# Optimization experiments

Measured on AMD Instinct MI355X. Metric: run time of the kernel, lower is better.

Reference implementation:

```python
import jax, jax.numpy as jnp
import numpy as np

EPS = 1e-5

def _conv(x, w, pad, groups=1):
    return jax.lax.conv_general_dilated(
        x, w, window_strides=(1, 1), padding=[(pad, pad), (pad, pad)],
        dimension_numbers=('NCHW', 'OIHW', 'NCHW'), feature_group_count=groups)

def _bn(x, g, b, m, v):
    # inference batch-norm, per-channel
    s = g * jax.lax.rsqrt(v + EPS)
    return x * s[None, :, None, None] + (b - m * s)[None, :, None, None]

def setup_inputs() -> dict:
    key = jax.random.key(0)
    ks = jax.random.split(key, 20)
    B, C, H, W = 32, 128, 64, 64
    cs = C // 2  # c_split = 64
    d = {
        'x': jax.random.normal(ks[0], (B, C, H, W), jnp.float32),
        'weights': jax.random.uniform(ks[1], (B, 2), jnp.float32),
        'indices': jax.random.randint(ks[2], (B, 2), 0, 4, jnp.int32),
        # expert 0: Conv(cs -> C, k=3, p=1) + BN + SiLU
        'e0_w': jax.random.normal(ks[3], (C, cs, 3, 3), jnp.float32) * 0.05,
        'e0_g': jax.random.uniform(ks[4], (C,), jnp.float32, 0.5, 1.5),
        'e0_b': jax.random.normal(ks[5], (C,), jnp.float32) * 0.1,
        'e0_m': jax.random.normal(ks[6], (C,), jnp.float32) * 0.1,
        'e0_v': jax.random.uniform(ks[7], (C,), jnp.float32, 0.5, 1.5),
        # expert 1: depthwise 5x5 (cs, groups=cs) -> 1x1 (cs -> C) -> BN -> SiLU
        'e1_dw': jax.random.normal(ks[8], (cs, 1, 5, 5), jnp.float32) * 0.05,
        'e1_pw': jax.random.normal(ks[9], (C, cs, 1, 1), jnp.float32) * 0.05,
        'e1_g': jax.random.uniform(ks[10], (C,), jnp.float32, 0.5, 1.5),
        'e1_b': jax.random.normal(ks[11], (C,), jnp.float32) * 0.1,
        'e1_m': jax.random.normal(ks[12], (C,), jnp.float32) * 0.1,
        'e1_v': jax.random.uniform(ks[13], (C,), jnp.float32, 0.5, 1.5),
        # expert 2: GhostConv(C -> C): cv1 = Conv(C, C//2, 3), cv2 = Conv(C//2, C//2, 5, groups=C//2)
        'e2a_w': jax.random.normal(ks[14], (cs, C, 3, 3), jnp.float32) * 0.05,
        'e2a_g': jax.random.uniform(ks[15], (cs,), jnp.float32, 0.5, 1.5),
        'e2a_b': jax.random.normal(ks[16], (cs,), jnp.float32) * 0.1,
        'e2a_m': jax.random.normal(ks[17], (cs,), jnp.float32) * 0.1,
        'e2a_v': jax.random.uniform(ks[18], (cs,), jnp.float32, 0.5, 1.5),
        'e2b_w': jax.random.normal(ks[19], (cs, 1, 5, 5), jnp.float32) * 0.05,
    }
    ks2 = jax.random.split(jax.random.key(1), 4)
    d['e2b_g'] = jax.random.uniform(ks2[0], (cs,), jnp.float32, 0.5, 1.5)
    d['e2b_b'] = jax.random.normal(ks2[1], (cs,), jnp.float32) * 0.1
    d['e2b_m'] = jax.random.normal(ks2[2], (cs,), jnp.float32) * 0.1
    d['e2b_v'] = jax.random.uniform(ks2[3], (cs,), jnp.float32, 0.5, 1.5)
    return d

def _forward(x, weights, indices,
             e0_w, e0_g, e0_b, e0_m, e0_v,
             e1_dw, e1_pw, e1_g, e1_b, e1_m, e1_v,
             e2a_w, e2a_g, e2a_b, e2a_m, e2a_v,
             e2b_w, e2b_g, e2b_b, e2b_m, e2b_v):
    C = x.shape[1]
    cs = C // 2
    x_rgb, x_ir = x[:, :cs], x[:, cs:]
    # expert outputs computed densely over the whole batch, masked combine below
    e0 = jax.nn.silu(_bn(_conv(x_rgb, e0_w, pad=1), e0_g, e0_b, e0_m, e0_v))
    e1 = jax.nn.silu(_bn(_conv(_conv(x_ir, e1_dw, pad=2, groups=cs), e1_pw, pad=0),
                         e1_g, e1_b, e1_m, e1_v))
    g1 = jax.nn.silu(_bn(_conv(x, e2a_w, pad=1), e2a_g, e2a_b, e2a_m, e2a_v))
    g2 = jax.nn.silu(_bn(_conv(g1, e2b_w, pad=2, groups=cs), e2b_g, e2b_b, e2b_m, e2b_v))
    e2 = jnp.concatenate([g1, g2], axis=1)
    out = jnp.zeros_like(x)
    K = indices.shape[1]
    for k in range(K):  # small fixed top-k loop
        idx = indices[:, k][:, None, None, None]          # [B,1,1,1]
        w = weights[:, k][:, None, None, None]            # [B,1,1,1]
        out = out + jnp.where(idx == 0, e0 * w, 0.0)
        out = out + jnp.where(idx == 1, e1 * w, 0.0)
        out = out + jnp.where(idx == 2, e2 * w, 0.0)
        out = out + jnp.where(idx == 3, x * 0.1, 0.0)
    return out

def reference(x, weights, indices,
              e0_w, e0_g, e0_b, e0_m, e0_v,
              e1_dw, e1_pw, e1_g, e1_b, e1_m, e1_v,
              e2a_w, e2a_g, e2a_b, e2a_m, e2a_v,
              e2b_w, e2b_g, e2b_b, e2b_m, e2b_v):
    return _forward(x, weights, indices,
                    e0_w, e0_g, e0_b, e0_m, e0_v,
                    e1_dw, e1_pw, e1_g, e1_b, e1_m, e1_v,
                    e2a_w, e2a_g, e2a_b, e2a_m, e2a_v,
                    e2b_w, e2b_g, e2b_b, e2b_m, e2b_v)
```

## Files before the change

kernel.cpp:

```cpp
#include <hip/hip_runtime.h>

#define B_  32
#define C_  128
#define CS  64
#define H_  64
#define W_  64
#define HW  (H_*W_)

typedef __attribute__((ext_vector_type(8))) short bf16x8_t;
typedef __attribute__((ext_vector_type(4))) float f32x4_t;
typedef unsigned short u16;
typedef unsigned int   u32;

__device__ __forceinline__ float silu_f(float v) { return v / (1.f + __expf(-v)); }

__device__ __forceinline__ u16 f2bf(float f) {
    u32 u = __float_as_uint(f);
    u = (u + 0x7FFFu + ((u >> 16) & 1u)) >> 16;
    return (u16)u;
}
__device__ __forceinline__ float bf2f(u16 u) {
    return __uint_as_float(((u32)u) << 16);
}
__device__ __forceinline__ u32 cvtpk(float a, float b) {
    u32 r;
    asm("v_cvt_pk_bf16_f32 %0, %1, %2" : "=v"(r) : "v"(a), "v"(b));
    return r;
}

__device__ __forceinline__ void get_coeffs(const float* __restrict__ wts,
                                           const int* __restrict__ idxs, int b,
                                           float& c0, float& c1, float& c2, float& cid) {
    int   i0 = idxs[b*2+0], i1 = idxs[b*2+1];
    float w0 = wts[b*2+0],  w1 = wts[b*2+1];
    c0  = (i0==0?w0:0.f)   + (i1==0?w1:0.f);
    c1  = (i0==1?w0:0.f)   + (i1==1?w1:0.f);
    c2  = (i0==2?w0:0.f)   + (i1==2?w1:0.f);
    cid = (i0==3?0.1f:0.f) + (i1==3?0.1f:0.f);
}

__global__ __launch_bounds__(256) void k_prep(
    const float* __restrict__ e0w, const float* __restrict__ e2aw, const float* __restrict__ e1pw,
    u16* __restrict__ Wt0f, u16* __restrict__ Wt2f, u16* __restrict__ Wt1f)
{
    const int i0 = blockIdx.x*256 + threadIdx.x, stride = gridDim.x*256;
    for (int i = i0; i < 73728; i += stride) {
        int j = i&7, lane = (i>>3)&63, cog = (i>>9)&7, kc = (i>>12)&1, tap = i>>13;
        int co = cog*16 + (lane&15), ci = kc*32 + (lane>>4)*8 + j;
        Wt0f[i] = f2bf(e0w[(size_t)(co*64 + ci)*9 + tap]);
    }
    for (int i = i0; i < 73728; i += stride) {
        int j = i&7, lane = (i>>3)&63, cog = (i>>9)&3, kc = (i>>11)&3, tap = i>>13;
        int co = cog*16 + (lane&15), ci = kc*32 + (lane>>4)*8 + j;
        Wt2f[i] = f2bf(e2aw[(size_t)(co*128 + ci)*9 + tap]);
    }
    for (int i = i0; i < 8192; i += stride) {
        int j = i&7, lane = (i>>3)&63, cog = (i>>9)&7, kc = (i>>12)&1;
        int co = cog*16 + (lane&15), ci = kc*32 + (lane>>4)*8 + j;
        Wt1f[i] = f2bf(e1pw[(size_t)co*64 + ci]);
    }
}

__device__ __forceinline__ void stage_x(
    const float* __restrict__ xb,
    char* lin, int orow0, int t)
{
    f32x4_t V0[8], V1[8];
    #pragma unroll
    for (int k = 0; k < 8; ++k) {
        const int u = t + k*256;
        const int quad = u & 15, r = (u >> 4) & 3, cp = u >> 6;
        const int hh = orow0 - 1 + r;
        const int hcl = (hh < 0) ? 0 : ((hh > 63) ? 63 : hh);
        const float* p0 = xb + (size_t)(2*cp)*HW + hcl*64 + quad*4;
        asm volatile("global_load_dwordx4 %0, %1, off" : "=v"(V0[k]) : "v"(p0));
        asm volatile("global_load_dwordx4 %0, %1, off" : "=v"(V1[k]) : "v"(p0 + HW));
    }
    asm volatile("s_waitcnt vmcnt(0)" ::: "memory");
    __builtin_amdgcn_sched_barrier(0);
    #pragma unroll
    for (int k = 0; k < 8; ++k) {
        const int u = t + k*256;
        const int quad = u & 15, r = (u >> 4) & 3, cp = u >> 6;
        const int hh = orow0 - 1 + r;
        const bool ok = (hh >= 0 && hh < H_);
        #pragma unroll
        for (int j = 0; j < 4; ++j) {
            const int p = r*66 + quad*4 + j + 1;
            const u32 a = ((u32)p*128 + (u32)cp*4) ^ (((u32)(p & 7)) << 4);
            float f0 = ok ? V0[k][j] : 0.f;
            float f1 = ok ? V1[k][j] : 0.f;
            *(u32*)(lin + a) = cvtpk(f0, f1);
        }
    }
    {
        const int cp = t & 31, side = (t >> 5) & 1, r = t >> 6;
        const int p = r*66 + side*65;
        const u32 a = ((u32)p*128 + (u32)cp*4) ^ (((u32)(p & 7)) << 4);
        *(u32*)(lin + a) = 0u;
    }
}

template<int NCF, int NPF, int TK, int COUT>
__device__ __forceinline__ void conv_pass(
    const char* lin, const u16* __restrict__ wb, int koff,
    int rbase, int pxbase, int l15, int kg,
    f32x4_t (&acc)[NCF][NPF])
{
    bf16x8_t A0[NCF], A1[NCF], A2[NCF];

    auto issueA = [&](int i, bf16x8_t (&dst)[NCF]) {
        const int tap = i >> 1, kcl = i & 1;
        const u16* wt = wb + (size_t)((tap*TK + koff + kcl)*(COUT/16))*512;
        #pragma unroll
        for (int cf = 0; cf < NCF; ++cf)
            asm volatile("global_load_dwordx4 %0, %1, off"
                         : "=v"(dst[cf]) : "v"(wt + ((size_t)cf << 9)));
    };
    auto ldsB = [&](int i, int pf) -> bf16x8_t {
        const int tap = i >> 1, kcl = i & 1;
        const int dh = tap / 3, dwp = tap % 3;
        const int p = (rbase + dh)*66 + pxbase + pf*16 + l15 + dwp;
        u32 a = (u32)p*128 + (u32)kcl*64 + (u32)kg*16;
        a ^= ((u32)(p & 7)) << 4;
        return *(const bf16x8_t*)(lin + a);
    };

    issueA(0, A0);
    issueA(1, A1);
    #pragma unroll
    for (int i = 0; i < 18; ++i) {
        if (i + 2 < 18) {
            const int s = (i + 2) % 3;
            if (s == 0)      issueA(i + 2, A0);
            else if (s == 1) issueA(i + 2, A1);
            else             issueA(i + 2, A2);
        }
        if (i < 16)       asm volatile("s_waitcnt vmcnt(8)" ::: "memory");
        else if (i == 16) asm volatile("s_waitcnt vmcnt(4)" ::: "memory");
        else              asm volatile("s_waitcnt vmcnt(0)" ::: "memory");
        __builtin_amdgcn_sched_barrier(0);
        bf16x8_t* ac = (i % 3 == 0) ? A0 : ((i % 3 == 1) ? A1 : A2);
        #pragma unroll
        for (int pf = 0; pf < NPF; ++pf) {
            bf16x8_t bfr = ldsB(i, pf);
            #pragma unroll
            for (int cf = 0; cf < NCF; ++cf)
                acc[cf][pf] = __builtin_amdgcn_mfma_f32_16x16x32_bf16(ac[cf], bfr, acc[cf][pf], 0, 0, 0);
        }
    }
}

__global__ __launch_bounds__(256, 3) void k_conv(
    const float* __restrict__ x,
    const float* __restrict__ wts, const int* __restrict__ idxs,
    const u16* __restrict__ Wt0f, const u16* __restrict__ Wt2f,
    const float* __restrict__ e0g, const float* __restrict__ e0b,
    const float* __restrict__ e0m, const float* __restrict__ e0v,
    const float* __restrict__ e2ag, const float* __restrict__ e2ab,
    const float* __restrict__ e2am, const float* __restrict__ e2av,
    const float* __restrict__ e1dw, const u16* __restrict__ Wt1f,
    const float* __restrict__ e1g, const float* __restrict__ e1b,
    const float* __restrict__ e1m, const float* __restrict__ e1v,
    float* __restrict__ out, u16* __restrict__ g1)
{
    __shared__ char uni[51968];
    const int b = blockIdx.y, orow0 = blockIdx.x*2, t = threadIdx.x;
    float c0, c1, c2, cid;
    get_coeffs(wts, idxs, b, c0, c1, c2, cid);

    const int lane = t & 63, l15 = lane & 15, kg = lane >> 4, wv = t >> 6;
    const float* xb = x + (size_t)b*C_*HW;

    if (blockIdx.z == 1) {
        if (c2 == 0.f) return;

        const int rw = wv >> 1, pw = wv & 1;
        const int pxbase = pw*32;
        f32x4_t acc[4][2];
        #pragma unroll
        for (int cf = 0; cf < 4; ++cf)
            #pragma unroll
            for (int pf = 0; pf < 2; ++pf)
                acc[cf][pf] = (f32x4_t){0.f, 0.f, 0.f, 0.f};

        const u16* wb = Wt2f + (size_t)lane*8;

        stage_x(xb, uni, orow0, t);
        __syncthreads();
        conv_pass<4, 2, 4, 64>(uni, wb, 0, rw, pxbase, l15, kg, acc);
        __syncthreads();
        stage_x(xb + (size_t)CS*HW, uni, orow0, t);
        __syncthreads();
        conv_pass<4, 2, 4, 64>(uni, wb, 2, rw, pxbase, l15, kg, acc);

        #pragma unroll
        for (int cf = 0; cf < 4; ++cf) {
            float sarr[4], tarr[4];
            #pragma unroll
            for (int r = 0; r < 4; ++r) {
                int co = cf*16 + kg*4 + r;
                float s = e2ag[co] * rsqrtf(e2av[co] + 1e-5f);
                sarr[r] = s; tarr[r] = e2ab[co] - e2am[co]*s;
            }
            #pragma unroll
            for (int pf = 0; pf < 2; ++pf) {
                size_t rowoff = (size_t)(orow0 + rw)*64 + pxbase + pf*16 + l15;
                #pragma unroll
                for (int r = 0; r < 4; ++r) {
                    int co = cf*16 + kg*4 + r;
                    float v = silu_f(acc[cf][pf][r]*sarr[r] + tarr[r]);
                    g1[((size_t)(b*CS+co))*HW + rowoff] = f2bf(v);
                }
            }
        }
        return;
    }

    const int cw = wv >> 1, rw = wv & 1;
    const int cobase = cw*64;

    if (c0 != 0.f) {
        stage_x(xb, uni, orow0, t);
        __syncthreads();

        f32x4_t acc[4][4];
        #pragma unroll
        for (int cf = 0; cf < 4; ++cf)
            #pragma unroll
            for (int pf = 0; pf < 4; ++pf)
                acc[cf][pf] = (f32x4_t){0.f, 0.f, 0.f, 0.f};

        const u16* wb = Wt0f + (size_t)(cobase >> 4)*512 + (size_t)lane*8;
        conv_pass<4, 4, 2, 128>(uni, wb, 0, rw, 0, l15, kg, acc);

        #pragma unroll
        for (int cf = 0; cf < 4; ++cf) {
            float sarr[4], tarr[4];
            #pragma unroll
            for (int r = 0; r < 4; ++r) {
                int co = cobase + cf*16 + kg*4 + r;
                float s = e0g[co] * rsqrtf(e0v[co] + 1e-5f);
                sarr[r] = s; tarr[r] = e0b[co] - e0m[co]*s;
            }
            #pragma unroll
            for (int pf = 0; pf < 4; ++pf) {
                size_t rowoff = (size_t)(orow0 + rw)*64 + pf*16 + l15;
                #pragma unroll
                for (int r = 0; r < 4; ++r) {
                    int co = cobase + cf*16 + kg*4 + r;
                    float v = silu_f(acc[cf][pf][r]*sarr[r] + tarr[r]);
                    size_t o = ((size_t)(b*C_+co))*HW + rowoff;
                    float idv = (cid != 0.f) ? cid*x[o] : 0.f;
                    out[o] = c0*v + idv;
                }
            }
        }
    } else if (c1 == 0.f) {
        for (int i = t; i < 4096; i += 256) {
            int ch = i >> 5, q = i & 31;
            size_t o = ((size_t)(b*C_+ch))*HW + (size_t)orow0*64 + q*4;
            float4 ov;
            if (cid != 0.f) {
                float4 xv = *(const float4*)(x + o);
                ov.x = cid*xv.x; ov.y = cid*xv.y; ov.z = cid*xv.z; ov.w = cid*xv.w;
            } else { ov.x = ov.y = ov.z = ov.w = 0.f; }
            *(float4*)(out + o) = ov;
        }
        return;
    } else {
        #pragma unroll
        for (int cf = 0; cf < 4; ++cf)
            #pragma unroll
            for (int pf = 0; pf < 4; ++pf) {
                size_t rowoff = (size_t)(orow0 + rw)*64 + pf*16 + l15;
                #pragma unroll
                for (int r = 0; r < 4; ++r) {
                    int co = cobase + cf*16 + kg*4 + r;
                    size_t o = ((size_t)(b*C_+co))*HW + rowoff;
                    out[o] = (cid != 0.f) ? cid*x[o] : 0.f;
                }
            }
    }

    if (c1 == 0.f) return;

    u16*   lin2 = (u16*)uni;
    u16*   lout = (u16*)(uni + 26880);
    float* wlf  = (float*)(uni + 45312);

    __syncthreads();
    for (int i = t; i < 64*25; i += 256) wlf[(i/25)*26 + (i%25)] = e1dw[i];

    #pragma unroll
    for (int pass = 0; pass < 2; ++pass) {
        if (pass) __syncthreads();
        for (int i = t; i < 6*32*16; i += 256) {
            int q = i & 15, chs = (i >> 4) & 31, r = i >> 9;
            int hh = orow0 - 2 + r;
            u32 w0 = 0u, w1 = 0u;
            if (hh >= 0 && hh < H_) {
                float4 v = *(const float4*)(x + ((size_t)(b*C_ + CS + pass*32 + chs))*HW + hh*64 + q*4);
                w0 = cvtpk(v.x, v.y); w1 = cvtpk(v.z, v.w);
            }
            u32* dst = (u32*)&lin2[(r*32 + chs)*70 + 2 + q*4];
            dst[0] = w0; dst[1] = w1;
        }
        for (int i = t; i < 6*32; i += 256) {
            int chs = i & 31, r = i >> 5;
            *(u32*)&lin2[(r*32 + chs)*70] = 0u;
            u32* e = (u32*)&lin2[(r*32 + chs)*70 + 66];
            e[0] = 0u; e[1] = 0u;
        }
        __syncthreads();

        {
            const int outrow = wv & 1, cgrp = wv >> 1;
            const int chloc = cgrp*16 + l15, cs_ = kg;
            const float* wch = &wlf[(pass*32 + chloc)*26];
            float accp[16];
            #pragma unroll
            for (int p = 0; p < 16; ++p) accp[p] = 0.f;
            #pragma unroll
            for (int kh = 0; kh < 5; ++kh) {
                const u16* src = &lin2[((outrow + kh)*32 + chloc)*70 + cs_*16];
                float rb[20];
                #pragma unroll
                for (int k = 0; k < 10; ++k) {
                    u32 u = *(const u32*)(src + 2*k);
                    rb[2*k]   = __uint_as_float(u << 16);
                    rb[2*k+1] = __uint_as_float(u & 0xFFFF0000u);
                }
                #pragma unroll
                for (int kw = 0; kw < 5; ++kw) {
                    float wvv = wch[kh*5 + kw];
                    #pragma unroll
                    for (int p = 0; p < 16; ++p) accp[p] += rb[p+kw]*wvv;
                }
            }
            const int px0 = outrow*64 + cs_*16;
            #pragma unroll
            for (int p = 0; p < 16; ++p)
                lout[(px0+p)*72 + pass*32 + chloc] = f2bf(accp[p]);
        }
    }
    __syncthreads();

    {
        const int pwv = rw;
        f32x4_t acc1[4][4];
        #pragma unroll
        for (int cf = 0; cf < 4; ++cf)
            #pragma unroll
            for (int pf = 0; pf < 4; ++pf)
                acc1[cf][pf] = (f32x4_t){0.f, 0.f, 0.f, 0.f};

        #pragma unroll
        for (int kc = 0; kc < 2; ++kc) {
            const u16* wt = Wt1f + (((size_t)(kc*8 + cw*4)) << 9) + lane*8;
            bf16x8_t af[4];
            #pragma unroll
            for (int cf = 0; cf < 4; ++cf) af[cf] = *(const bf16x8_t*)(wt + (cf << 9));
            const int k0 = kc*32 + kg*8;
            #pragma unroll
            for (int pf = 0; pf < 4; ++pf) {
                bf16x8_t bfr = *(const bf16x8_t*)&lout[(pwv*64 + pf*16 + l15)*72 + k0];
                #pragma unroll
                for (int cf = 0; cf < 4; ++cf)
                    acc1[cf][pf] = __builtin_amdgcn_mfma_f32_16x16x32_bf16(af[cf], bfr, acc1[cf][pf], 0, 0, 0);
            }
        }

        #pragma unroll
        for (int cf = 0; cf < 4; ++cf) {
            float sarr[4], tarr[4];
            #pragma unroll
            for (int r = 0; r < 4; ++r) {
                int co = cw*64 + cf*16 + kg*4 + r;
                float s = e1g[co] * rsqrtf(e1v[co] + 1e-5f);
                sarr[r] = s; tarr[r] = e1b[co] - e1m[co]*s;
            }
            #pragma unroll
            for (int pf = 0; pf < 4; ++pf) {
                size_t rowoff = (size_t)(orow0 + pwv)*64 + pf*16 + l15;
                #pragma unroll
                for (int r = 0; r < 4; ++r) {
                    int co = cw*64 + cf*16 + kg*4 + r;
                    float v = silu_f(acc1[cf][pf][r]*sarr[r] + tarr[r]);
                    out[((size_t)(b*C_+co))*HW + rowoff] += c1*v;
                }
            }
        }
    }
}

__global__ __launch_bounds__(256) void k_e2b(
    const u16* __restrict__ g1, const float* __restrict__ wts, const int* __restrict__ idxs,
    const float* __restrict__ dww, const float* __restrict__ gg, const float* __restrict__ bb,
    const float* __restrict__ mm, const float* __restrict__ vv, float* __restrict__ out)
{
    const int b = blockIdx.y, band = blockIdx.x, t = threadIdx.x;
    const int orow0 = band*2;

    float c0, c1, c2, cid;
    get_coeffs(wts, idxs, b, c0, c1, c2, cid);
    if (c2 == 0.f) return;

    __shared__ u16  lin[6*64*70];
    __shared__ float wl[64*26];

    for (int i = t; i < 64*25; i += 256) wl[(i/25)*26 + (i%25)] = dww[i];
    for (int i = t; i < 6*64*16; i += 256) {
        int q = i & 15, ch = (i >> 4) & 63, r = i >> 10;
        int hh = orow0 - 2 + r;
        u32 w0 = 0u, w1 = 0u;
        if (hh >= 0 && hh < H_) {
            const u32* src = (const u32*)(g1 + ((size_t)(b*CS+ch))*HW + hh*64 + q*4);
            w0 = src[0]; w1 = src[1];
        }
        u32* dst = (u32*)&lin[(r*64 + ch)*70 + 2 + q*4];
        dst[0] = w0; dst[1] = w1;
    }
    for (int i = t; i < 6*64; i += 256) {
        int ch = i & 63, r = i >> 6;
        *(u32*)&lin[(r*64 + ch)*70] = 0u;
        u32* e = (u32*)&lin[(r*64 + ch)*70 + 66];
        e[0] = 0u; e[1] = 0u;
    }
    __syncthreads();

    for (int i = t; i < 2*64*16; i += 256) {
        int q = i & 15, ch = (i >> 4) & 63, r = i >> 10;
        const u16* src = &lin[((r+2)*64 + ch)*70 + 2 + q*4];
        float* op = out + ((size_t)(b*C_+ch))*HW + (size_t)(orow0+r)*64 + q*4;
        float4 ov = *(float4*)op;
        ov.x += c2*bf2f(src[0]); ov.y += c2*bf2f(src[1]);
        ov.z += c2*bf2f(src[2]); ov.w += c2*bf2f(src[3]);
        *(float4*)op = ov;
    }

    const int lane = t & 63, chl = lane & 15, cs = lane >> 4;
    const int wv = t >> 6, outrow = wv & 1, chhalf = wv >> 1;

    #pragma unroll
    for (int chi = 0; chi < 2; ++chi) {
        const int ch = chhalf*32 + chl + chi*16;
        const float* wch = &wl[ch*26];
        float accp[16];
        #pragma unroll
        for (int p = 0; p < 16; ++p) accp[p] = 0.f;
        #pragma unroll
        for (int kh = 0; kh < 5; ++kh) {
            const u16* src = &lin[((outrow + kh)*64 + ch)*70 + cs*16];
            float rb[20];
            #pragma unroll
            for (int k = 0; k < 10; ++k) {
                u32 u = *(const u32*)(src + 2*k);
                rb[2*k]   = __uint_as_float(u << 16);
                rb[2*k+1] = __uint_as_float(u & 0xFFFF0000u);
            }
            #pragma unroll
            for (int kw = 0; kw < 5; ++kw) {
                float wvv = wch[kh*5 + kw];
                #pragma unroll
                for (int p = 0; p < 16; ++p) accp[p] += rb[p+kw]*wvv;
            }
        }
        float s = gg[ch] * rsqrtf(vv[ch] + 1e-5f);
        float tt = bb[ch] - mm[ch]*s;
        float* op = out + ((size_t)(b*C_ + CS + ch))*HW + (size_t)(orow0+outrow)*64 + cs*16;
        #pragma unroll
        for (int q = 0; q < 4; ++q) {
            float4 ov = *(float4*)(op + q*4);
            ov.x += c2*silu_f(accp[q*4+0]*s + tt);
            ov.y += c2*silu_f(accp[q*4+1]*s + tt);
            ov.z += c2*silu_f(accp[q*4+2]*s + tt);
            ov.w += c2*silu_f(accp[q*4+3]*s + tt);
            *(float4*)(op + q*4) = ov;
        }
    }
}

extern "C" void kernel_launch(void* const* d_in, const int* in_sizes, int n_in,
                              void* d_out, int out_size, void* d_ws, size_t ws_size,
                              hipStream_t stream) {
    const float* x    = (const float*)d_in[0];
    const float* wts  = (const float*)d_in[1];
    const int*   idxs = (const int*)  d_in[2];
    const float* e0w  = (const float*)d_in[3];
    const float* e0g  = (const float*)d_in[4];
    const float* e0b  = (const float*)d_in[5];
    const float* e0m  = (const float*)d_in[6];
    const float* e0v  = (const float*)d_in[7];
    const float* e1dw = (const float*)d_in[8];
    const float* e1pw = (const float*)d_in[9];
    const float* e1g  = (const float*)d_in[10];
    const float* e1b  = (const float*)d_in[11];
    const float* e1m  = (const float*)d_in[12];
    const float* e1v  = (const float*)d_in[13];
    const float* e2aw = (const float*)d_in[14];
    const float* e2ag = (const float*)d_in[15];
    const float* e2ab = (const float*)d_in[16];
    const float* e2am = (const float*)d_in[17];
    const float* e2av = (const float*)d_in[18];
    const float* e2bw = (const float*)d_in[19];
    const float* e2bg = (const float*)d_in[20];
    const float* e2bb = (const float*)d_in[21];
    const float* e2bm = (const float*)d_in[22];
    const float* e2bv = (const float*)d_in[23];

    float* out = (float*)d_out;

    u16* g1   = (u16*)d_ws;
    u16* Wt0f = g1 + (size_t)8388608;
    u16* Wt2f = Wt0f + 73728;
    u16* Wt1f = Wt2f + 73728;

    k_prep<<<128, 256, 0, stream>>>(e0w, e2aw, e1pw, Wt0f, Wt2f, Wt1f);
    k_conv<<<dim3(32, B_, 2), 256, 0, stream>>>(
        x, wts, idxs, Wt0f, Wt2f,
        e0g, e0b, e0m, e0v, e2ag, e2ab, e2am, e2av,
        e1dw, Wt1f, e1g, e1b, e1m, e1v, out, g1);
    k_e2b<<<dim3(32, B_), 256, 0, stream>>>(
        g1, wts, idxs, e2bw, e2bg, e2bb, e2bm, e2bv, out);
}
```

Baseline: 93.01 us.

## Shrink LDS footprint by staging depthwise convs in smaller channel passes

```diff
diff --git a/kernel.cpp b/kernel.cpp
--- a/kernel.cpp
+++ b/kernel.cpp
@@ -164,7 +164,7 @@
     const float* __restrict__ e1m, const float* __restrict__ e1v,
     float* __restrict__ out, u16* __restrict__ g1)
 {
-    __shared__ char uni[51968];
+    __shared__ char uni[33792];
     const int b = blockIdx.y, orow0 = blockIdx.x*2, t = threadIdx.x;
     float c0, c1, c2, cid;
     get_coeffs(wts, idxs, b, c0, c1, c2, cid);
@@ -285,12 +285,133 @@
 
     if (c1 == 0.f) return;
 
-    u16*   lin2 = (u16*)uni;
-    u16*   lout = (u16*)(uni + 26880);
-    float* wlf  = (float*)(uni + 45312);
+    u16*   lin4 = (u16*)uni;
+    u16*   lout = (u16*)(uni + 13440);
+    float* wlf  = (float*)(uni + 31872);
 
     __syncthreads();
-    for (int i = t; i < 64*25; i += 256) wlf[(i/25)*26 + (i%25)] = e1dw[i];
+
+    #pragma unroll
+    for (int pass = 0; pass < 4; ++pass) {
+        if (pass) __syncthreads();
+        for (int i = t; i < 6*16*16; i += 256) {
+            int q = i & 15, chs = (i >> 4) & 15, r = i >> 8;
+            int hh = orow0 - 2 + r;
+            u32 w0 = 0u, w1 = 0u;
+            if (hh >= 0 && hh < H_) {
+                float4 v = *(const float4*)(x + ((size_t)(b*C_ + CS + pass*16 + chs))*HW + hh*64 + q*4);
+                w0 = cvtpk(v.x, v.y); w1 = cvtpk(v.z, v.w);
+            }
+            u32* dst = (u32*)&lin4[(r*16 + chs)*70 + 2 + q*4];
+            dst[0] = w0; dst[1] = w1;
+        }
+        for (int i = t; i < 6*16; i += 256) {
+            int chs = i & 15, r = i >> 4;
+            *(u32*)&lin4[(r*16 + chs)*70] = 0u;
+            u32* e = (u32*)&lin4[(r*16 + chs)*70 + 66];
+            e[0] = 0u; e[1] = 0u;
+        }
+        for (int i = t; i < 16*25; i += 256)
+            wlf[(i/25)*26 + (i%25)] = e1dw[pass*16*25 + i];
+        __syncthreads();
+
+        {
+            const int outrow = wv & 1, pxhalf = wv >> 1;
+            const int chloc = l15;
+            const int px0 = pxhalf*32 + kg*8;
+            const float* wch = &wlf[chloc*26];
+            float accp[8];
+            #pragma unroll
+            for (int p = 0; p < 8; ++p) accp[p] = 0.f;
+            #pragma unroll
+            for (int kh = 0; kh < 5; ++kh) {
+                const u16* src = &lin4[((outrow + kh)*16 + chloc)*70 + px0];
+                float rb[12];
+                #pragma unroll
+                for (int k = 0; k < 6; ++k) {
+                    u32 u = *(const u32*)(src + 2*k);
+                    rb[2*k]   = __uint_as_float(u << 16);
+                    rb[2*k+1] = __uint_as_float(u & 0xFFFF0000u);
+                }
+                #pragma unroll
+                for (int kw = 0; kw < 5; ++kw) {
+                    float wvv = wch[kh*5 + kw];
+                    #pragma unroll
+                    for (int p = 0; p < 8; ++p) accp[p] += rb[p+kw]*wvv;
+                }
+            }
+            #pragma unroll
+            for (int p = 0; p < 8; ++p)
+                lout[(outrow*64 + px0 + p)*72 + pass*16 + chloc] = f2bf(accp[p]);
+        }
+    }
+    __syncthreads();
+
+    {
+        const int pwv = rw;
+        f32x4_t acc1[4][4];
+        #pragma unroll
+        for (int cf = 0; cf < 4; ++cf)
+            #pragma unroll
+            for (int pf = 0; pf < 4; ++pf)
+                acc1[cf][pf] = (f32x4_t){0.f, 0.f, 0.f, 0.f};
+
+        #pragma unroll
+        for (int kc = 0; kc < 2; ++kc) {
+            const u16* wt = Wt1f + (((size_t)(kc*8 + cw*4)) << 9) + lane*8;
+            bf16x8_t af[4];
+            #pragma unroll
+            for (int cf = 0; cf < 4; ++cf) af[cf] = *(const bf16x8_t*)(wt + (cf << 9));
+            const int k0 = kc*32 + kg*8;
+            #pragma unroll
+            for (int pf = 0; pf < 4; ++pf) {
+                bf16x8_t bfr = *(const bf16x8_t*)&lout[(pwv*64 + pf*16 + l15)*72 + k0];
+                #pragma unroll
+                for (int cf = 0; cf < 4; ++cf)
+                    acc1[cf][pf] = __builtin_amdgcn_mfma_f32_16x16x32_bf16(af[cf], bfr, acc1[cf][pf], 0, 0, 0);
+            }
+        }
+
+        #pragma unroll
+        for (int cf = 0; cf < 4; ++cf) {
+            float sarr[4], tarr[4];
+            #pragma unroll
+            for (int r = 0; r < 4; ++r) {
+                int co = cw*64 + cf*16 + kg*4 + r;
+                float s = e1g[co] * rsqrtf(e1v[co] + 1e-5f);
+                sarr[r] = s; tarr[r] = e1b[co] - e1m[co]*s;
+            }
+            #pragma unroll
+            for (int pf = 0; pf < 4; ++pf) {
+                size_t rowoff = (size_t)(orow0 + pwv)*64 + pf*16 + l15;
+                #pragma unroll
+                for (int r = 0; r < 4; ++r) {
+                    int co = cw*64 + cf*16 + kg*4 + r;
+                    float v = silu_f(acc1[cf][pf][r]*sarr[r] + tarr[r]);
+                    out[((size_t)(b*C_+co))*HW + rowoff] += c1*v;
+                }
+            }
+        }
+    }
+}
+
+__global__ __launch_bounds__(256) void k_e2b(
+    const u16* __restrict__ g1, const float* __restrict__ wts, const int* __restrict__ idxs,
+    const float* __restrict__ dww, const float* __restrict__ gg, const float* __restrict__ bb,
+    const float* __restrict__ mm, const float* __restrict__ vv, float* __restrict__ out)
+{
+    const int b = blockIdx.y, band = blockIdx.x, t = threadIdx.x;
+    const int orow0 = band*2;
+
+    float c0, c1, c2, cid;
+    get_coeffs(wts, idxs, b, c0, c1, c2, cid);
+    if (c2 == 0.f) return;
+
+    __shared__ u16  lin32[6*32*70];
+    __shared__ float wl32[32*26];
+
+    const int lane = t & 63, l15 = lane & 15, kg = lane >> 4;
+    const int wv = t >> 6, outrow = wv & 1, cg = wv >> 1;
 
     #pragma unroll
     for (int pass = 0; pass < 2; ++pass) {
@@ -300,30 +421,41 @@
             int hh = orow0 - 2 + r;
             u32 w0 = 0u, w1 = 0u;
             if (hh >= 0 && hh < H_) {
-                float4 v = *(const float4*)(x + ((size_t)(b*C_ + CS + pass*32 + chs))*HW + hh*64 + q*4);
-                w0 = cvtpk(v.x, v.y); w1 = cvtpk(v.z, v.w);
-            }
-            u32* dst = (u32*)&lin2[(r*32 + chs)*70 + 2 + q*4];
+                const u32* src = (const u32*)(g1 + ((size_t)(b*CS + pass*32 + chs))*HW + hh*64 + q*4);
+                w0 = src[0]; w1 = src[1];
+            }
+            u32* dst = (u32*)&lin32[(r*32 + chs)*70 + 2 + q*4];
             dst[0] = w0; dst[1] = w1;
         }
         for (int i = t; i < 6*32; i += 256) {
             int chs = i & 31, r = i >> 5;
-            *(u32*)&lin2[(r*32 + chs)*70] = 0u;
-            u32* e = (u32*)&lin2[(r*32 + chs)*70 + 66];
+            *(u32*)&lin32[(r*32 + chs)*70] = 0u;
+            u32* e = (u32*)&lin32[(r*32 + chs)*70 + 66];
             e[0] = 0u; e[1] = 0u;
         }
+        for (int i = t; i < 32*25; i += 256)
+            wl32[(i/25)*26 + (i%25)] = dww[pass*32*25 + i];
         __syncthreads();
 
+        for (int i = t; i < 2*32*16; i += 256) {
+            int q = i & 15, chs = (i >> 4) & 31, r = i >> 9;
+            const u16* src = &lin32[((r+2)*32 + chs)*70 + 2 + q*4];
+            float* op = out + ((size_t)(b*C_ + pass*32 + chs))*HW + (size_t)(orow0+r)*64 + q*4;
+            float4 ov = *(float4*)op;
+            ov.x += c2*bf2f(src[0]); ov.y += c2*bf2f(src[1]);
+            ov.z += c2*bf2f(src[2]); ov.w += c2*bf2f(src[3]);
+            *(float4*)op = ov;
+        }
+
         {
-            const int outrow = wv & 1, cgrp = wv >> 1;
-            const int chloc = cgrp*16 + l15, cs_ = kg;
-            const float* wch = &wlf[(pass*32 + chloc)*26];
+            const int chloc = cg*16 + l15;
+            const float* wch = &wl32[chloc*26];
             float accp[16];
             #pragma unroll
             for (int p = 0; p < 16; ++p) accp[p] = 0.f;
             #pragma unroll
             for (int kh = 0; kh < 5; ++kh) {
-                const u16* src = &lin2[((outrow + kh)*32 + chloc)*70 + cs_*16];
+                const u16* src = &lin32[((outrow + kh)*32 + chloc)*70 + kg*16];
                 float rb[20];
                 #pragma unroll
                 for (int k = 0; k < 10; ++k) {
@@ -338,145 +470,19 @@
                     for (int p = 0; p < 16; ++p) accp[p] += rb[p+kw]*wvv;
                 }
             }
-            const int px0 = outrow*64 + cs_*16;
-            #pragma unroll
-            for (int p = 0; p < 16; ++p)
-                lout[(px0+p)*72 + pass*32 + chloc] = f2bf(accp[p]);
-        }
-    }
-    __syncthreads();
-
-    {
-        const int pwv = rw;
-        f32x4_t acc1[4][4];
-        #pragma unroll
-        for (int cf = 0; cf < 4; ++cf)
-            #pragma unroll
-            for (int pf = 0; pf < 4; ++pf)
-                acc1[cf][pf] = (f32x4_t){0.f, 0.f, 0.f, 0.f};
-
-        #pragma unroll
-        for (int kc = 0; kc < 2; ++kc) {
-            const u16* wt = Wt1f + (((size_t)(kc*8 + cw*4)) << 9) + lane*8;
-            bf16x8_t af[4];
-            #pragma unroll
-            for (int cf = 0; cf < 4; ++cf) af[cf] = *(const bf16x8_t*)(wt + (cf << 9));
-            const int k0 = kc*32 + kg*8;
-            #pragma unroll
-            for (int pf = 0; pf < 4; ++pf) {
-                bf16x8_t bfr = *(const bf16x8_t*)&lout[(pwv*64 + pf*16 + l15)*72 + k0];
-                #pragma unroll
-                for (int cf = 0; cf < 4; ++cf)
-                    acc1[cf][pf] = __builtin_amdgcn_mfma_f32_16x16x32_bf16(af[cf], bfr, acc1[cf][pf], 0, 0, 0);
-            }
-        }
-
-        #pragma unroll
-        for (int cf = 0; cf < 4; ++cf) {
-            float sarr[4], tarr[4];
-            #pragma unroll
-            for (int r = 0; r < 4; ++r) {
-                int co = cw*64 + cf*16 + kg*4 + r;
-                float s = e1g[co] * rsqrtf(e1v[co] + 1e-5f);
-                sarr[r] = s; tarr[r] = e1b[co] - e1m[co]*s;
-            }
-            #pragma unroll
-            for (int pf = 0; pf < 4; ++pf) {
-                size_t rowoff = (size_t)(orow0 + pwv)*64 + pf*16 + l15;
-                #pragma unroll
-                for (int r = 0; r < 4; ++r) {
-                    int co = cw*64 + cf*16 + kg*4 + r;
-                    float v = silu_f(acc1[cf][pf][r]*sarr[r] + tarr[r]);
-                    out[((size_t)(b*C_+co))*HW + rowoff] += c1*v;
-                }
-            }
-        }
-    }
-}
-
-__global__ __launch_bounds__(256) void k_e2b(
-    const u16* __restrict__ g1, const float* __restrict__ wts, const int* __restrict__ idxs,
-    const float* __restrict__ dww, const float* __restrict__ gg, const float* __restrict__ bb,
-    const float* __restrict__ mm, const float* __restrict__ vv, float* __restrict__ out)
-{
-    const int b = blockIdx.y, band = blockIdx.x, t = threadIdx.x;
-    const int orow0 = band*2;
-
-    float c0, c1, c2, cid;
-    get_coeffs(wts, idxs, b, c0, c1, c2, cid);
-    if (c2 == 0.f) return;
-
-    __shared__ u16  lin[6*64*70];
-    __shared__ float wl[64*26];
-
-    for (int i = t; i < 64*25; i += 256) wl[(i/25)*26 + (i%25)] = dww[i];
-    for (int i = t; i < 6*64*16; i += 256) {
-        int q = i & 15, ch = (i >> 4) & 63, r = i >> 10;
-        int hh = orow0 - 2 + r;
-        u32 w0 = 0u, w1 = 0u;
-        if (hh >= 0 && hh < H_) {
-            const u32* src = (const u32*)(g1 + ((size_t)(b*CS+ch))*HW + hh*64 + q*4);
-            w0 = src[0]; w1 = src[1];
-        }
-        u32* dst = (u32*)&lin[(r*64 + ch)*70 + 2 + q*4];
-        dst[0] = w0; dst[1] = w1;
-    }
-    for (int i = t; i < 6*64; i += 256) {
-        int ch = i & 63, r = i >> 6;
-        *(u32*)&lin[(r*64 + ch)*70] = 0u;
-        u32* e = (u32*)&lin[(r*64 + ch)*70 + 66];
-        e[0] = 0u; e[1] = 0u;
-    }
-    __syncthreads();
-
-    for (int i = t; i < 2*64*16; i += 256) {
-        int q = i & 15, ch = (i >> 4) & 63, r = i >> 10;
-        const u16* src = &lin[((r+2)*64 + ch)*70 + 2 + q*4];
-        float* op = out + ((size_t)(b*C_+ch))*HW + (size_t)(orow0+r)*64 + q*4;
-        float4 ov = *(float4*)op;
-        ov.x += c2*bf2f(src[0]); ov.y += c2*bf2f(src[1]);
-        ov.z += c2*bf2f(src[2]); ov.w += c2*bf2f(src[3]);
-        *(float4*)op = ov;
-    }
-
-    const int lane = t & 63, chl = lane & 15, cs = lane >> 4;
-    const int wv = t >> 6, outrow = wv & 1, chhalf = wv >> 1;
-
-    #pragma unroll
-    for (int chi = 0; chi < 2; ++chi) {
-        const int ch = chhalf*32 + chl + chi*16;
-        const float* wch = &wl[ch*26];
-        float accp[16];
-        #pragma unroll
-        for (int p = 0; p < 16; ++p) accp[p] = 0.f;
-        #pragma unroll
-        for (int kh = 0; kh < 5; ++kh) {
-            const u16* src = &lin[((outrow + kh)*64 + ch)*70 + cs*16];
-            float rb[20];
-            #pragma unroll
-            for (int k = 0; k < 10; ++k) {
-                u32 u = *(const u32*)(src + 2*k);
-                rb[2*k]   = __uint_as_float(u << 16);
-                rb[2*k+1] = __uint_as_float(u & 0xFFFF0000u);
-            }
-            #pragma unroll
-            for (int kw = 0; kw < 5; ++kw) {
-                float wvv = wch[kh*5 + kw];
-                #pragma unroll
-                for (int p = 0; p < 16; ++p) accp[p] += rb[p+kw]*wvv;
-            }
-        }
-        float s = gg[ch] * rsqrtf(vv[ch] + 1e-5f);
-        float tt = bb[ch] - mm[ch]*s;
-        float* op = out + ((size_t)(b*C_ + CS + ch))*HW + (size_t)(orow0+outrow)*64 + cs*16;
-        #pragma unroll
-        for (int q = 0; q < 4; ++q) {
-            float4 ov = *(float4*)(op + q*4);
-            ov.x += c2*silu_f(accp[q*4+0]*s + tt);
-            ov.y += c2*silu_f(accp[q*4+1]*s + tt);
-            ov.z += c2*silu_f(accp[q*4+2]*s + tt);
-            ov.w += c2*silu_f(accp[q*4+3]*s + tt);
-            *(float4*)(op + q*4) = ov;
+            const int chg = pass*32 + chloc;
+            float s = gg[chg] * rsqrtf(vv[chg] + 1e-5f);
+            float tt = bb[chg] - mm[chg]*s;
+            float* op = out + ((size_t)(b*C_ + CS + chg))*HW + (size_t)(orow0+outrow)*64 + kg*16;
+            #pragma unroll
+            for (int q = 0; q < 4; ++q) {
+                float4 ov = *(float4*)(op + q*4);
+                ov.x += c2*silu_f(accp[q*4+0]*s + tt);
+                ov.y += c2*silu_f(accp[q*4+1]*s + tt);
+                ov.z += c2*silu_f(accp[q*4+2]*s + tt);
+                ov.w += c2*silu_f(accp[q*4+3]*s + tt);
+                *(float4*)(op + q*4) = ov;
+            }
         }
     }
 }
```

Measured after the change: 94.49 us. Within noise of the previous version (+1.6%).
